# Kernel tuning notes

Hardware: AMD Instinct MI355X
Metric: run time of the kernel (lower is better)

Reference implementation:

```python
import jax, jax.numpy as jnp
import numpy as np

N_NODES = 100000
N_EDGES = 3200000
IN_CH = 128
HID_CH = 128
OUT_CH = 64
N_GRAPHS = 128


def gcn_conv(x, edge_index, edge_weight, W, b):
    # x: [N, F_in]; edge_index: [2, E] (row=source j, col=target i); edge_weight: [E]
    N = x.shape[0]
    x = x @ W  # [N, F_out]
    # add self-loops with weight 1 (PyG GCNConv default, fill_value=1.0)
    loop = jnp.arange(N, dtype=edge_index.dtype)
    row = jnp.concatenate([edge_index[0], loop])
    col = jnp.concatenate([edge_index[1], loop])
    w = jnp.concatenate([edge_weight, jnp.ones((N,), dtype=x.dtype)])
    # symmetric normalization: deg computed at target (col)
    deg = jax.ops.segment_sum(w, col, num_segments=N)
    dinv = jnp.where(deg > 0, jax.lax.rsqrt(deg), 0.0)
    norm = dinv[row] * w * dinv[col]  # [E+N]
    msg = x[row] * norm[:, None]  # gather + scale
    out = jax.ops.segment_sum(msg, col, num_segments=N)  # scatter-add
    return out + b


def setup_inputs() -> dict:
    key = jax.random.key(0)
    ks = jax.random.split(key, 10)
    x = jax.random.normal(ks[0], (N_NODES, IN_CH), dtype=jnp.float32)
    edge_index = jax.random.randint(ks[1], (2, N_EDGES), 0, N_NODES, dtype=jnp.int64)
    edge_attr = jax.random.uniform(ks[2], (N_EDGES,), dtype=jnp.float32)
    batch = jnp.sort(jax.random.randint(ks[3], (N_NODES,), 0, N_GRAPHS, dtype=jnp.int64))
    # GCNConv weights (glorot) and zero bias, classifier xavier_normal + bias 0.1
    def glorot(k, fi, fo):
        s = jnp.sqrt(6.0 / (fi + fo))
        return jax.random.uniform(k, (fi, fo), minval=-s, maxval=s, dtype=jnp.float32)
    W1 = glorot(ks[4], IN_CH, HID_CH)
    b1 = jnp.zeros((HID_CH,), dtype=jnp.float32)
    W2 = glorot(ks[5], HID_CH, HID_CH)
    b2 = jnp.zeros((HID_CH,), dtype=jnp.float32)
    std = jnp.sqrt(2.0 / (HID_CH + OUT_CH))
    Wc = jax.random.normal(ks[6], (HID_CH, OUT_CH), dtype=jnp.float32) * std
    bc = jnp.full((OUT_CH,), 0.1, dtype=jnp.float32)
    return {"x": x, "edge_index": edge_index, "edge_attr": edge_attr,
            "batch": batch, "W1": W1, "b1": b1, "W2": W2, "b2": b2,
            "Wc": Wc, "bc": bc}


def reference(x, edge_index, edge_attr, batch, W1, b1, W2, b2, Wc, bc):
    h = jax.nn.relu(gcn_conv(x, edge_index, edge_attr, W1, b1))
    h = jax.nn.relu(gcn_conv(h, edge_index, edge_attr, W2, b2))
    pooled = jax.ops.segment_sum(h, batch, num_segments=N_GRAPHS)  # [G, HID]
    logits = pooled @ Wc + bc
    return jax.nn.sigmoid(logits)
```

## Files before the change

### kernel.cpp

```cpp
#include <hip/hip_runtime.h>
#include <hip/hip_bf16.h>
#include <hip/hip_fp16.h>


#define FEAT 128
#define OUTC 64
#define NB_SHIFT 8
#define BINSZ 256
#define CAP 9216
#define TILE_A 8192
#define CNT_STRIDE 16
#define LDW 136

typedef _Float16 half8 __attribute__((ext_vector_type(8)));
typedef float    f32x4 __attribute__((ext_vector_type(4)));
typedef int      iv2  __attribute__((ext_vector_type(2)));
typedef int      iv4  __attribute__((ext_vector_type(4)));

__global__ __launch_bounds__(256) void bin_edges(const int* __restrict__ ei,
                                                 const float* __restrict__ ew,
                                                 int* __restrict__ binCnt,
                                                 int2* __restrict__ binned,
                                                 int E, int nbins) {
    __shared__ int hist[512];
    __shared__ int base[512];
    int tid = threadIdx.x;
    int e0 = blockIdx.x * TILE_A;
    for (int i = tid; i < nbins; i += 256) hist[i] = 0;
    __syncthreads();
    for (int i = 0; i < TILE_A; i += 256) {
        int e = e0 + i + tid;
        if (e < E) atomicAdd(&hist[ei[E + e] >> NB_SHIFT], 1);
    }
    __syncthreads();
    for (int i = tid; i < nbins; i += 256) {
        int h = hist[i];
        base[i] = (h > 0) ? atomicAdd(&binCnt[i * CNT_STRIDE], h) : 0;
        hist[i] = 0;
    }
    __syncthreads();
    for (int i = 0; i < TILE_A; i += 256) {
        int e = e0 + i + tid;
        if (e < E) {
            int col = ei[E + e];
            int row = ei[e];
            float w = ew[e];
            int b  = col >> NB_SHIFT;
            int lp = atomicAdd(&hist[b], 1);
            int pos = base[b] + lp;
            if (pos < CAP) {
                int cl = col & (BINSZ - 1);
                binned[(size_t)b * CAP + pos] = make_int2((cl << 24) | row, __float_as_int(w));
            }
        }
    }
}

__global__ __launch_bounds__(256) void bin_sort_csr(int2* __restrict__ binned,
                                                    const int* __restrict__ binCnt,
                                                    int* __restrict__ offs,
                                                    int* __restrict__ cnt,
                                                    float* __restrict__ dinv, int N) {
    extern __shared__ int2 sE[];
    __shared__ float dsum[BINSZ];
    __shared__ int kh[BINSZ], kb[BINSZ], ksc[BINSZ];
    int tid = threadIdx.x, b = blockIdx.x;
    int node0 = b << NB_SHIFT;
    dsum[tid] = 0.f;
    kh[tid] = 0;
    __syncthreads();
    int ne = min(binCnt[b * CNT_STRIDE], CAP);
    int2* src = binned + (size_t)b * CAP;
    for (int i = tid; i < ne; i += 256) {
        int2 m = src[i];
        int cl = ((unsigned)m.x) >> 24;
        atomicAdd(&kh[cl], 1);
        unsafeAtomicAdd(&dsum[cl], __int_as_float(m.y));
    }
    __syncthreads();
    int v = kh[tid];
    ksc[tid] = v;
    __syncthreads();
    for (int off = 1; off < BINSZ; off <<= 1) {
        int t = (tid >= off) ? ksc[tid - off] : 0;
        __syncthreads();
        ksc[tid] += t;
        __syncthreads();
    }
    kb[tid] = ksc[tid] - v;
    kh[tid] = 0;
    __syncthreads();
    for (int i = tid; i < ne; i += 256) {
        int2 m = src[i];
        int cl = ((unsigned)m.x) >> 24;
        int p = kb[cl] + atomicAdd(&kh[cl], 1);
        unsigned short hs = __half_as_ushort(__float2half(__int_as_float(m.y)));
        sE[p] = make_int2(m.x & 0xFFFFFF, (int)hs | ((int)hs << 16));
    }
    __syncthreads();
    for (int i = tid; i < ne; i += 256) src[i] = sE[i];
    int node = node0 + tid;
    if (node < N) {
        offs[node] = b * CAP + kb[tid];
        cnt[node]  = kh[tid];
        dinv[node] = rsqrtf(1.0f + dsum[tid]);
    }
}

__global__ void wt_prep(const float* __restrict__ W, _Float16* __restrict__ Wt) {
    int i = blockIdx.x * 256 + threadIdx.x;
    int n = i >> 7, k = i & 127;
    Wt[(size_t)n * LDW + k] = (_Float16)W[(size_t)k * FEAT + n];
}

template<typename TIn>
__global__ __launch_bounds__(256) void gemm_mfma(const TIn* __restrict__ X,
                                                 const _Float16* __restrict__ Wt,
                                                 const float* __restrict__ dinv,
                                                 __half* __restrict__ Y, int N) {
    __shared__ _Float16 sWt[FEAT * LDW];
    int tid  = threadIdx.x;
    int row0 = blockIdx.x * 128;
    {
        const int4* src = (const int4*)Wt;
        int4* dst = (int4*)sWt;
        for (int i = tid; i < (FEAT * LDW) / 8; i += 256) dst[i] = src[i];
    }
    __syncthreads();

    int wave = tid >> 6;
    int lane = tid & 63;
    int m    = lane & 15;
    int quad = lane >> 4;

    f32x4 acc[2][8];
    #pragma unroll
    for (int rt = 0; rt < 2; ++rt)
        #pragma unroll
        for (int ct = 0; ct < 8; ++ct)
            acc[rt][ct] = (f32x4){0.f, 0.f, 0.f, 0.f};

    int rowA[2];
    rowA[0] = min(row0 + wave * 32 + m, N - 1);
    rowA[1] = min(row0 + wave * 32 + 16 + m, N - 1);

    #pragma unroll
    for (int kt = 0; kt < 4; ++kt) {
        int k0 = kt * 32;
        half8 a[2];
        #pragma unroll
        for (int rt = 0; rt < 2; ++rt) {
            if constexpr (sizeof(TIn) == 4) {
                const float4* p = (const float4*)((const float*)X + (size_t)rowA[rt] * FEAT + k0 + quad * 8);
                float4 f0 = p[0], f1 = p[1];
                half8 h;
                h[0] = (_Float16)f0.x; h[1] = (_Float16)f0.y;
                h[2] = (_Float16)f0.z; h[3] = (_Float16)f0.w;
                h[4] = (_Float16)f1.x; h[5] = (_Float16)f1.y;
                h[6] = (_Float16)f1.z; h[7] = (_Float16)f1.w;
                a[rt] = h;
            } else {
                a[rt] = *(const half8*)((const _Float16*)X + (size_t)rowA[rt] * FEAT + k0 + quad * 8);
            }
        }
        #pragma unroll
        for (int ct = 0; ct < 8; ++ct) {
            half8 b = *(const half8*)&sWt[(ct * 16 + m) * LDW + k0 + quad * 8];
            acc[0][ct] = __builtin_amdgcn_mfma_f32_16x16x32_f16(a[0], b, acc[0][ct], 0, 0, 0);
            acc[1][ct] = __builtin_amdgcn_mfma_f32_16x16x32_f16(a[1], b, acc[1][ct], 0, 0, 0);
        }
    }

    #pragma unroll
    for (int rt = 0; rt < 2; ++rt) {
        int lr0 = wave * 32 + rt * 16 + quad * 4;
        #pragma unroll
        for (int r = 0; r < 4; ++r) {
            int gr = row0 + lr0 + r;
            if (gr < N) {
                float d = dinv[gr];
                #pragma unroll
                for (int ct = 0; ct < 8; ++ct)
                    Y[(size_t)gr * FEAT + ct * 16 + m] = __float2half(d * acc[rt][ct][r]);
            }
        }
    }
}

__global__ __launch_bounds__(256) void agg_kernel(const __half* __restrict__ Y,
                                                  const int2* __restrict__ elist,
                                                  const int* __restrict__ offs,
                                                  const int* __restrict__ cnt,
                                                  const float* __restrict__ dinv,
                                                  const float* __restrict__ bias,
                                                  __half* __restrict__ Out, int N) {
    int node = blockIdx.x * 4 + (threadIdx.x >> 6);
    int lane = threadIdx.x & 63;
    if (node >= N) return;
    int grp = lane >> 4;
    int fl  = lane & 15;
    int c = cnt[node];
    const iv2* meta = (const iv2*)(elist + offs[node]);

    __half2 z = __floats2half2_rn(0.f, 0.f);
    __half2 a0 = z, a1 = z, a2 = z, a3 = z;
    __half2 b0 = z, b1 = z, b2 = z, b3 = z;

    if (grp == 0) {
        int4 sv = ((const int4*)(Y + (size_t)node * FEAT))[fl];
        a0 = *(const __half2*)&sv.x; a1 = *(const __half2*)&sv.y;
        a2 = *(const __half2*)&sv.z; a3 = *(const __half2*)&sv.w;
    }

    for (int t = 0; t < c; t += 8) {
        int eA = t + grp;
        int eB = t + 4 + grp;
        iv2 mA = (eA < c) ? __builtin_nontemporal_load(meta + eA) : (iv2){node, 0};
        iv2 mB = (eB < c) ? __builtin_nontemporal_load(meta + eB) : (iv2){node, 0};
        int4 vA = *(const int4*)(Y + (size_t)mA.x * FEAT + fl * 8);
        int4 vB = *(const int4*)(Y + (size_t)mB.x * FEAT + fl * 8);
        int wAi = mA.y, wBi = mB.y;
        __half2 wA = *(const __half2*)&wAi;
        __half2 wB = *(const __half2*)&wBi;
        a0 = __hfma2(wA, *(const __half2*)&vA.x, a0);
        a1 = __hfma2(wA, *(const __half2*)&vA.y, a1);
        a2 = __hfma2(wA, *(const __half2*)&vA.z, a2);
        a3 = __hfma2(wA, *(const __half2*)&vA.w, a3);
        b0 = __hfma2(wB, *(const __half2*)&vB.x, b0);
        b1 = __hfma2(wB, *(const __half2*)&vB.y, b1);
        b2 = __hfma2(wB, *(const __half2*)&vB.z, b2);
        b3 = __hfma2(wB, *(const __half2*)&vB.w, b3);
    }

    float2 F0 = __half22float2(a0), F1 = __half22float2(a1);
    float2 F2 = __half22float2(a2), F3 = __half22float2(a3);
    {
        float2 t0 = __half22float2(b0), t1 = __half22float2(b1);
        float2 t2 = __half22float2(b2), t3 = __half22float2(b3);
        F0.x += t0.x; F0.y += t0.y; F1.x += t1.x; F1.y += t1.y;
        F2.x += t2.x; F2.y += t2.y; F3.x += t3.x; F3.y += t3.y;
    }
    float f[8] = {F0.x, F0.y, F1.x, F1.y, F2.x, F2.y, F3.x, F3.y};
    #pragma unroll
    for (int i = 0; i < 8; ++i) {
        f[i] += __shfl_xor(f[i], 16);
        f[i] += __shfl_xor(f[i], 32);
    }
    if (grp == 0) {
        float d = dinv[node];
        int c0 = fl * 8;
        float4 bo0 = *(const float4*)(bias + c0);
        float4 bo1 = *(const float4*)(bias + c0 + 4);
        __half2 p01 = __floats2half2_rn(fmaxf(d * f[0] + bo0.x, 0.f), fmaxf(d * f[1] + bo0.y, 0.f));
        __half2 p23 = __floats2half2_rn(fmaxf(d * f[2] + bo0.z, 0.f), fmaxf(d * f[3] + bo0.w, 0.f));
        __half2 p45 = __floats2half2_rn(fmaxf(d * f[4] + bo1.x, 0.f), fmaxf(d * f[5] + bo1.y, 0.f));
        __half2 p67 = __floats2half2_rn(fmaxf(d * f[6] + bo1.z, 0.f), fmaxf(d * f[7] + bo1.w, 0.f));
        iv4 ov = { *(int*)&p01, *(int*)&p23, *(int*)&p45, *(int*)&p67 };
        __builtin_nontemporal_store(ov, (iv4*)(Out + (size_t)node * FEAT + c0));
    }
}

__global__ void pool_kernel(const __half* __restrict__ H, const int* __restrict__ batch,
                            float* __restrict__ pooled, int N, int chunk) {
    int f  = threadIdx.x;
    int n0 = blockIdx.x * chunk;
    if (n0 >= N) return;
    int n1 = min(n0 + chunk, N);
    float acc = 0.f;
    int cur = batch[n0];
    for (int n = n0; n < n1; ++n) {
        int g = batch[n];
        if (g != cur) {
            unsafeAtomicAdd(&pooled[cur * FEAT + f], acc);
            acc = 0.f;
            cur = g;
        }
        unsigned short us = __builtin_nontemporal_load((const unsigned short*)(H + (size_t)n * FEAT + f));
        acc += __half2float(__ushort_as_half(us));
    }
    unsafeAtomicAdd(&pooled[cur * FEAT + f], acc);
}

__global__ void classify_kernel(const float* __restrict__ pooled, const float* __restrict__ Wc,
                                const float* __restrict__ bc, float* __restrict__ out) {
    int g = blockIdx.x;
    int c = threadIdx.x;
    float acc = bc[c];
    const float* pr = pooled + g * FEAT;
    for (int k = 0; k < FEAT; ++k) acc += pr[k] * Wc[k * OUTC + c];
    out[g * OUTC + c] = 1.0f / (1.0f + expf(-acc));
}

extern "C" void kernel_launch(void* const* d_in, const int* in_sizes, int n_in,
                              void* d_out, int out_size, void* d_ws, size_t ws_size,
                              hipStream_t stream) {
    const float* x     = (const float*)d_in[0];
    const int*   ei    = (const int*)d_in[1];
    const float* ew    = (const float*)d_in[2];
    const int*   batch = (const int*)d_in[3];
    const float* W1    = (const float*)d_in[4];
    const float* b1    = (const float*)d_in[5];
    const float* W2    = (const float*)d_in[6];
    const float* b2    = (const float*)d_in[7];
    const float* Wc    = (const float*)d_in[8];
    const float* bc    = (const float*)d_in[9];
    float* out = (float*)d_out;

    const int N = in_sizes[0] / FEAT;
    const int E = in_sizes[2];
    const int G = out_size / OUTC;
    const int nbins = (N + BINSZ - 1) / BINSZ;

    char* w = (char*)d_ws;
    size_t off = 0;
    auto alloc = [&](size_t bytes) {
        void* p = w + off;
        off = (off + bytes + 255) & ~(size_t)255;
        return p;
    };
    float*     dinv   = (float*)alloc((size_t)N * 4);
    int*       cnt    = (int*)alloc((size_t)N * 4);
    int*       offs   = (int*)alloc((size_t)N * 4);
    int*       binCnt = (int*)alloc((size_t)nbins * CNT_STRIDE * 4);
    int2*      binned = (int2*)alloc((size_t)nbins * CAP * 8);
    __half*    bufY   = (__half*)alloc((size_t)N * FEAT * 2);
    __half*    bufH   = (__half*)alloc((size_t)N * FEAT * 2);
    float*     pooled = (float*)alloc((size_t)G * FEAT * 4);
    _Float16*  wt1    = (_Float16*)alloc((size_t)FEAT * LDW * 2);
    _Float16*  wt2    = (_Float16*)alloc((size_t)FEAT * LDW * 2);
    (void)ws_size;

    hipMemsetAsync(binCnt, 0, (size_t)nbins * CNT_STRIDE * 4, stream);
    hipMemsetAsync(pooled, 0, (size_t)G * FEAT * 4, stream);

    bin_edges<<<(E + TILE_A - 1) / TILE_A, 256, 0, stream>>>(ei, ew, binCnt, binned, E, nbins);
    bin_sort_csr<<<nbins, 256, (size_t)CAP * sizeof(int2), stream>>>(binned, binCnt, offs, cnt, dinv, N);
    wt_prep<<<64, 256, 0, stream>>>(W1, wt1);
    wt_prep<<<64, 256, 0, stream>>>(W2, wt2);

    const int gemm_blocks = (N + 127) / 128;
    const int agg_blocks  = (N + 3) / 4;

    gemm_mfma<float><<<gemm_blocks, 256, 0, stream>>>(x, wt1, dinv, bufY, N);
    agg_kernel<<<agg_blocks, 256, 0, stream>>>(bufY, binned, offs, cnt, dinv, b1, bufH, N);
    gemm_mfma<__half><<<gemm_blocks, 256, 0, stream>>>(bufH, wt2, dinv, bufY, N);
    agg_kernel<<<agg_blocks, 256, 0, stream>>>(bufY, binned, offs, cnt, dinv, b2, bufH, N);

    const int chunk = 128;
    pool_kernel<<<(N + chunk - 1) / chunk, FEAT, 0, stream>>>(bufH, batch, pooled, N, chunk);
    classify_kernel<<<G, OUTC, 0, stream>>>(pooled, Wc, bc, out);
}
```

Before: 564.7 us.

## Stage binned edges in LDS and write them to global memory in coalesced runs

Result: faster. 510.7 us (-9.6%).

```diff
diff --git a/kernel.cpp b/kernel.cpp
--- a/kernel.cpp
+++ b/kernel.cpp
@@ -14,7 +14,6 @@
 
 typedef _Float16 half8 __attribute__((ext_vector_type(8)));
 typedef float    f32x4 __attribute__((ext_vector_type(4)));
-typedef int      iv2  __attribute__((ext_vector_type(2)));
 typedef int      iv4  __attribute__((ext_vector_type(4)));
 
 __global__ __launch_bounds__(256) void bin_edges(const int* __restrict__ ei,
@@ -22,37 +21,54 @@
                                                  int* __restrict__ binCnt,
                                                  int2* __restrict__ binned,
                                                  int E, int nbins) {
-    __shared__ int hist[512];
-    __shared__ int base[512];
+    extern __shared__ int2 sE[];
+    __shared__ int kh[512], kb[512], kc[512], kg[512], ksc[512];
     int tid = threadIdx.x;
     int e0 = blockIdx.x * TILE_A;
-    for (int i = tid; i < nbins; i += 256) hist[i] = 0;
+    kh[tid] = 0; kh[tid + 256] = 0;
+    kc[tid] = 0; kc[tid + 256] = 0;
     __syncthreads();
     for (int i = 0; i < TILE_A; i += 256) {
         int e = e0 + i + tid;
-        if (e < E) atomicAdd(&hist[ei[E + e] >> NB_SHIFT], 1);
-    }
-    __syncthreads();
-    for (int i = tid; i < nbins; i += 256) {
-        int h = hist[i];
-        base[i] = (h > 0) ? atomicAdd(&binCnt[i * CNT_STRIDE], h) : 0;
-        hist[i] = 0;
-    }
+        if (e < E) atomicAdd(&kh[ei[E + e] >> NB_SHIFT], 1);
+    }
+    __syncthreads();
+    int v0 = kh[tid], v1 = kh[tid + 256];
+    ksc[tid] = v0; ksc[tid + 256] = v1;
+    __syncthreads();
+    for (int off = 1; off < 512; off <<= 1) {
+        int a0 = (tid >= off) ? ksc[tid - off] : 0;
+        int a1 = (tid + 256 >= off) ? ksc[tid + 256 - off] : 0;
+        __syncthreads();
+        ksc[tid] += a0; ksc[tid + 256] += a1;
+        __syncthreads();
+    }
+    kb[tid] = ksc[tid] - v0;
+    kb[tid + 256] = ksc[tid + 256] - v1;
+    if (tid < nbins && v0 > 0) kg[tid] = atomicAdd(&binCnt[tid * CNT_STRIDE], v0);
+    int t2 = tid + 256;
+    if (t2 < nbins && v1 > 0) kg[t2] = atomicAdd(&binCnt[t2 * CNT_STRIDE], v1);
     __syncthreads();
     for (int i = 0; i < TILE_A; i += 256) {
         int e = e0 + i + tid;
         if (e < E) {
             int col = ei[E + e];
             int row = ei[e];
-            float w = ew[e];
-            int b  = col >> NB_SHIFT;
-            int lp = atomicAdd(&hist[b], 1);
-            int pos = base[b] + lp;
-            if (pos < CAP) {
-                int cl = col & (BINSZ - 1);
-                binned[(size_t)b * CAP + pos] = make_int2((cl << 24) | row, __float_as_int(w));
-            }
-        }
+            unsigned short hs = __half_as_ushort(__float2half(ew[e]));
+            int b = col >> NB_SHIFT;
+            int p = kb[b] + atomicAdd(&kc[b], 1);
+            int cl = col & (BINSZ - 1);
+            sE[p] = make_int2((cl << 24) | row, (b << 16) | (int)hs);
+        }
+    }
+    __syncthreads();
+    int tot = ksc[511];
+    for (int i = tid; i < tot; i += 256) {
+        int2 m = sE[i];
+        int b = ((unsigned)m.y) >> 16;
+        int loc = kg[b] + (i - kb[b]);
+        if (loc < CAP)
+            binned[(size_t)b * CAP + loc] = make_int2(m.x, m.y & 0xFFFF);
     }
 }
 
@@ -75,7 +91,7 @@
         int2 m = src[i];
         int cl = ((unsigned)m.x) >> 24;
         atomicAdd(&kh[cl], 1);
-        unsafeAtomicAdd(&dsum[cl], __int_as_float(m.y));
+        unsafeAtomicAdd(&dsum[cl], __half2float(__ushort_as_half((unsigned short)(m.y & 0xFFFF))));
     }
     __syncthreads();
     int v = kh[tid];
@@ -94,8 +110,8 @@
         int2 m = src[i];
         int cl = ((unsigned)m.x) >> 24;
         int p = kb[cl] + atomicAdd(&kh[cl], 1);
-        unsigned short hs = __half_as_ushort(__float2half(__int_as_float(m.y)));
-        sE[p] = make_int2(m.x & 0xFFFFFF, (int)hs | ((int)hs << 16));
+        int hw = m.y & 0xFFFF;
+        sE[p] = make_int2(m.x & 0xFFFFFF, hw | (hw << 16));
     }
     __syncthreads();
     for (int i = tid; i < ne; i += 256) src[i] = sE[i];
@@ -200,7 +216,7 @@
     int grp = lane >> 4;
     int fl  = lane & 15;
     int c = cnt[node];
-    const iv2* meta = (const iv2*)(elist + offs[node]);
+    const int2* meta = elist + offs[node];
 
     __half2 z = __floats2half2_rn(0.f, 0.f);
     __half2 a0 = z, a1 = z, a2 = z, a3 = z;
@@ -215,13 +231,12 @@
     for (int t = 0; t < c; t += 8) {
         int eA = t + grp;
         int eB = t + 4 + grp;
-        iv2 mA = (eA < c) ? __builtin_nontemporal_load(meta + eA) : (iv2){node, 0};
-        iv2 mB = (eB < c) ? __builtin_nontemporal_load(meta + eB) : (iv2){node, 0};
+        int2 mA = (eA < c) ? meta[eA] : make_int2(node, 0);
+        int2 mB = (eB < c) ? meta[eB] : make_int2(node, 0);
         int4 vA = *(const int4*)(Y + (size_t)mA.x * FEAT + fl * 8);
         int4 vB = *(const int4*)(Y + (size_t)mB.x * FEAT + fl * 8);
-        int wAi = mA.y, wBi = mB.y;
-        __half2 wA = *(const __half2*)&wAi;
-        __half2 wB = *(const __half2*)&wBi;
+        __half2 wA = *(const __half2*)&mA.y;
+        __half2 wB = *(const __half2*)&mB.y;
         a0 = __hfma2(wA, *(const __half2*)&vA.x, a0);
         a1 = __hfma2(wA, *(const __half2*)&vA.y, a1);
         a2 = __hfma2(wA, *(const __half2*)&vA.z, a2);
@@ -256,7 +271,7 @@
         __half2 p45 = __floats2half2_rn(fmaxf(d * f[4] + bo1.x, 0.f), fmaxf(d * f[5] + bo1.y, 0.f));
         __half2 p67 = __floats2half2_rn(fmaxf(d * f[6] + bo1.z, 0.f), fmaxf(d * f[7] + bo1.w, 0.f));
         iv4 ov = { *(int*)&p01, *(int*)&p23, *(int*)&p45, *(int*)&p67 };
-        __builtin_nontemporal_store(ov, (iv4*)(Out + (size_t)node * FEAT + c0));
+        *(iv4*)(Out + (size_t)node * FEAT + c0) = ov;
     }
 }
 
@@ -275,8 +290,7 @@
             acc = 0.f;
             cur = g;
         }
-        unsigned short us = __builtin_nontemporal_load((const unsigned short*)(H + (size_t)n * FEAT + f));
-        acc += __half2float(__ushort_as_half(us));
+        acc += __half2float(H[(size_t)n * FEAT + f]);
     }
     unsafeAtomicAdd(&pooled[cur * FEAT + f], acc);
 }
@@ -333,7 +347,7 @@
     hipMemsetAsync(binCnt, 0, (size_t)nbins * CNT_STRIDE * 4, stream);
     hipMemsetAsync(pooled, 0, (size_t)G * FEAT * 4, stream);
 
-    bin_edges<<<(E + TILE_A - 1) / TILE_A, 256, 0, stream>>>(ei, ew, binCnt, binned, E, nbins);
+    bin_edges<<<(E + TILE_A - 1) / TILE_A, 256, (size_t)TILE_A * sizeof(int2), stream>>>(ei, ew, binCnt, binned, E, nbins);
     bin_sort_csr<<<nbins, 256, (size_t)CAP * sizeof(int2), stream>>>(binned, binCnt, offs, cnt, dinv, N);
     wt_prep<<<64, 256, 0, stream>>>(W1, wt1);
     wt_prep<<<64, 256, 0, stream>>>(W2, wt2);
```
